# Kernel optimization log

Hardware: AMD Instinct MI355X
Metric: run time of the kernel (lower is better)

The kernel has to match this reference:

```python
import jax, jax.numpy as jnp
import numpy as np

N_EXPERTS = 8
K_ACTIVE = 2
D_MODEL = 512
D_FF = 2048
T = 4096  # batch * seq_len


def _xavier(key, shape, fan_in, fan_out):
    limit = np.sqrt(6.0 / (fan_in + fan_out))
    return jax.random.uniform(key, shape, jnp.float32, -limit, limit)


def setup_inputs() -> dict:
    key = jax.random.key(0)
    k1, k2, k3, k4, k5 = jax.random.split(key, 5)
    hidden_states = jax.random.normal(k1, (T, D_MODEL), jnp.float32)
    selected_experts = jax.random.randint(k2, (T, K_ACTIVE), 0, N_EXPERTS, jnp.int64)
    expert_masks = jax.random.uniform(k3, (T, N_EXPERTS), jnp.float32)
    # stacked expert weights; torch Linear computes x @ W.T, we store [E, in, out]
    W1 = _xavier(k4, (N_EXPERTS, D_MODEL, D_FF), D_MODEL, D_FF)
    W2 = _xavier(k5, (N_EXPERTS, D_FF, D_MODEL), D_FF, D_MODEL)
    return {
        "hidden_states": hidden_states,
        "selected_experts": selected_experts,
        "expert_masks": expert_masks,
        "W1": W1,
        "W2": W2,
    }


def reference(hidden_states, selected_experts, expert_masks, W1, W2):
    # hidden_states: [T, d_model]; selected_experts: [T, k]; W1: [E, d, f]; W2: [E, f, d]
    t, d = hidden_states.shape
    n_experts = W1.shape[0]
    k = selected_experts.shape[1]

    expert_outputs = jnp.zeros((t, k, d), dtype=hidden_states.dtype)
    for e in range(n_experts):  # fixed small expert set
        h = jax.nn.gelu(hidden_states @ W1[e], approximate=False)  # [T, d_ff]
        y = h @ W2[e]                                              # [T, d_model]
        mask = selected_experts == e                               # [T, k]; each (t,slot) matches exactly one e
        expert_outputs = jnp.where(mask[..., None], y[:, None, :], expert_outputs)

    # expert_loads[e] = (# (token, slot) assignments to e) / T, matching the torch loop
    flat = selected_experts.reshape(-1)
    expert_loads = jnp.zeros((n_experts,), jnp.float32).at[flat].add(1.0) / t
    return expert_outputs, expert_loads
```

## Files before the change

### kernel.cpp

```cpp
#include <hip/hip_runtime.h>
#include <hip/hip_bf16.h>


typedef __bf16 bf16x8 __attribute__((ext_vector_type(8)));
typedef float f32x4 __attribute__((ext_vector_type(4)));

#define DM 512
#define DF 2048
#define NE 8
#define NTOK 4096
#define NPAIR 8192
#define HCAP 9216

__device__ __forceinline__ unsigned short f2bf(float x) {
    unsigned u = __builtin_bit_cast(unsigned, x);
    return (unsigned short)((u + 0x7fffu + ((u >> 16) & 1u)) >> 16);
}
__device__ __forceinline__ unsigned pack2(float lo, float hi) {
    return (unsigned)f2bf(lo) | ((unsigned)f2bf(hi) << 16);
}
__device__ __forceinline__ float gelu_fast(float x) {
    float x2 = x * x;
    float z = x * __builtin_fmaf(x2, -0.1029432f, -2.3022083f);
    float e = __builtin_amdgcn_exp2f(z);
    return x * __builtin_amdgcn_rcpf(1.0f + e);
}
__device__ __forceinline__ void dma16(const unsigned short* g, unsigned short* l) {
    __builtin_amdgcn_global_load_lds(
        (const __attribute__((address_space(1))) void*)g,
        (__attribute__((address_space(3))) void*)l, 16, 0, 0);
}
__device__ __forceinline__ int slot64(int row, int c) { return row * 8 + (c ^ (row & 7)); }

__device__ __forceinline__ void mfma_step(const unsigned short* Ab, const unsigned short* Bb,
                                          int wm, int wn, int quad, int l15,
                                          f32x4 (&acc)[4][4]) {
#pragma unroll
    for (int kk = 0; kk < 2; ++kk) {
        const int c = kk * 4 + quad;
        bf16x8 a[4], b[4];
#pragma unroll
        for (int fm = 0; fm < 4; ++fm) {
            int row = wm * 64 + fm * 16 + l15;
            a[fm] = __builtin_bit_cast(bf16x8, *(const uint4*)&Ab[slot64(row, c) * 8]);
        }
#pragma unroll
        for (int fn = 0; fn < 4; ++fn) {
            int row = wn * 64 + fn * 16 + l15;
            b[fn] = __builtin_bit_cast(bf16x8, *(const uint4*)&Bb[slot64(row, c) * 8]);
        }
#pragma unroll
        for (int fm = 0; fm < 4; ++fm)
#pragma unroll
            for (int fn = 0; fn < 4; ++fn)
                acc[fm][fn] = __builtin_amdgcn_mfma_f32_16x16x32_bf16(a[fm], b[fn], acc[fm][fn], 0, 0, 0);
    }
}

#define STAGE(buf, ko)                                        \
    do {                                                      \
        _Pragma("unroll") for (int j_ = 0; j_ < 4; ++j_) {    \
            dma16(ga[j_] + (ko), la[j_] + (buf) * 8192);      \
            dma16(gb[j_] + (ko), lb[j_] + (buf) * 8192);      \
        }                                                     \
    } while (0)

#define WAITN(n)                                                  \
    do {                                                          \
        __builtin_amdgcn_sched_barrier(0);                        \
        asm volatile("s_waitcnt vmcnt(" #n ")" ::: "memory");     \
        __builtin_amdgcn_sched_barrier(0);                        \
    } while (0)

#define BAR() __builtin_amdgcn_s_barrier()

__global__ void k_prep(const float* __restrict__ X, unsigned short* __restrict__ Xb,
                       const float* __restrict__ W1, unsigned short* __restrict__ W1T,
                       const float* __restrict__ W2, unsigned short* __restrict__ W2T,
                       const int* __restrict__ sel, int* __restrict__ counts_g,
                       int* __restrict__ opad_g, int* __restrict__ rowmap,
                       float* __restrict__ loads_out) {
    __shared__ unsigned short T[64][65];
    __shared__ int hist[NE], cur[NE], off[NE];
    const int b = blockIdx.x, tid = threadIdx.x;

    if (b < 1024) {
        int i = (b * 256 + tid) * 8;
        float4 a = *(const float4*)(X + i);
        float4 c = *(const float4*)(X + i + 4);
        uint4 u;
        u.x = pack2(a.x, a.y); u.y = pack2(a.z, a.w);
        u.z = pack2(c.x, c.y); u.w = pack2(c.z, c.w);
        *(uint4*)(Xb + i) = u;
    } else if (b < 3072) {
        const int t = b - 1024;
        const int bx = t & 31, by = (t >> 5) & 7, bz = t >> 8;
        const int tx = tid & 15, ty = tid >> 4;
        const int r0 = by * 64, c0 = bx * 64;
        const float* src = W1 + ((size_t)bz * DM + r0) * DF + c0;
#pragma unroll
        for (int i = 0; i < 4; ++i) {
            int r = ty + i * 16;
            float4 v = *(const float4*)(src + (size_t)r * DF + tx * 4);
            T[tx * 4 + 0][r] = f2bf(v.x); T[tx * 4 + 1][r] = f2bf(v.y);
            T[tx * 4 + 2][r] = f2bf(v.z); T[tx * 4 + 3][r] = f2bf(v.w);
        }
        __syncthreads();
        unsigned short* dst = W1T + ((size_t)bz * DF + c0) * DM + r0;
#pragma unroll
        for (int i = 0; i < 4; ++i) {
            int c = ty + i * 16;
            ushort4 w;
            w.x = T[c][tx * 4 + 0]; w.y = T[c][tx * 4 + 1];
            w.z = T[c][tx * 4 + 2]; w.w = T[c][tx * 4 + 3];
            *(ushort4*)(dst + (size_t)c * DM + tx * 4) = w;
        }
    } else if (b == 3072) {
        if (tid < NE) { hist[tid] = 0; cur[tid] = 0; }
        __syncthreads();
#pragma unroll
        for (int i = 0; i < NPAIR / 256; ++i)
            atomicAdd(&hist[sel[i * 256 + tid]], 1);
        __syncthreads();
        if (tid == 0) {
            int s = 0;
            for (int e = 0; e < NE; ++e) {
                off[e] = s;
                s += (hist[e] + 127) & ~127;
                counts_g[e] = hist[e];
                opad_g[e] = off[e];
                loads_out[e] = (float)hist[e] * (1.0f / (float)NTOK);
            }
        }
        __syncthreads();
#pragma unroll
        for (int i = 0; i < NPAIR / 256; ++i) {
            int p = i * 256 + tid;
            int e = sel[p];
            int pos = atomicAdd(&cur[e], 1);
            rowmap[off[e] + pos] = p;
        }
    } else {
        const int t = b - 3073;
        const int bx = t & 7, by = (t >> 3) & 31, bz = t >> 8;
        const int tx = tid & 15, ty = tid >> 4;
        const int r0 = by * 64, c0 = bx * 64;
        const float* src = W2 + ((size_t)bz * DF + r0) * DM + c0;
#pragma unroll
        for (int i = 0; i < 4; ++i) {
            int r = ty + i * 16;
            float4 v = *(const float4*)(src + (size_t)r * DM + tx * 4);
            T[tx * 4 + 0][r] = f2bf(v.x); T[tx * 4 + 1][r] = f2bf(v.y);
            T[tx * 4 + 2][r] = f2bf(v.z); T[tx * 4 + 3][r] = f2bf(v.w);
        }
        __syncthreads();
        unsigned short* dst = W2T + ((size_t)bz * DM + c0) * DF + r0;
#pragma unroll
        for (int i = 0; i < 4; ++i) {
            int c = ty + i * 16;
            ushort4 w;
            w.x = T[c][tx * 4 + 0]; w.y = T[c][tx * 4 + 1];
            w.z = T[c][tx * 4 + 2]; w.w = T[c][tx * 4 + 3];
            *(ushort4*)(dst + (size_t)c * DF + tx * 4) = w;
        }
    }
}

__global__ void k_tw2(const float* __restrict__ in, unsigned short* __restrict__ out) {
    __shared__ unsigned short T[64][65];
    const int tid = threadIdx.x;
    const int tx = tid & 15, ty = tid >> 4;
    const int r0 = blockIdx.y * 64, c0 = blockIdx.x * 64;
    const float* src = in + ((size_t)blockIdx.z * DF + r0) * DM + c0;
#pragma unroll
    for (int i = 0; i < 4; ++i) {
        int r = ty + i * 16;
        float4 v = *(const float4*)(src + (size_t)r * DM + tx * 4);
        T[tx * 4 + 0][r] = f2bf(v.x); T[tx * 4 + 1][r] = f2bf(v.y);
        T[tx * 4 + 2][r] = f2bf(v.z); T[tx * 4 + 3][r] = f2bf(v.w);
    }
    __syncthreads();
    unsigned short* dst = out + ((size_t)blockIdx.z * DM + c0) * DF + r0;
#pragma unroll
    for (int i = 0; i < 4; ++i) {
        int c = ty + i * 16;
        ushort4 w;
        w.x = T[c][tx * 4 + 0]; w.y = T[c][tx * 4 + 1];
        w.z = T[c][tx * 4 + 2]; w.w = T[c][tx * 4 + 3];
        *(ushort4*)(dst + (size_t)c * DF + tx * 4) = w;
    }
}

__launch_bounds__(256, 2)
__global__ void k_gemm1d(const unsigned short* __restrict__ Xb,
                         const unsigned short* __restrict__ W1T,
                         const int* __restrict__ counts, const int* __restrict__ opad,
                         const int* __restrict__ rowmap, unsigned short* __restrict__ H) {
    const int e = blockIdx.z, mt = blockIdx.y, nt = blockIdx.x;
    const int grow = opad[e] + mt * 128;
    int valid = counts[e] - mt * 128;
    if (valid <= 0) return;
    if (valid > 128) valid = 128;

    __shared__ __align__(16) unsigned short SM[4][8192];
    __shared__ int toks[128];

    const int tid = threadIdx.x;
    if (tid < 128) {
        int i = (tid < valid) ? tid : 0;
        toks[tid] = rowmap[grow + i] >> 1;
    }
    __syncthreads();

    const int wave = tid >> 6, lane = tid & 63;
    const int wm = wave >> 1, wn = wave & 1;
    const int quad = lane >> 4, l15 = lane & 15;

    const unsigned short* ga[4];
    const unsigned short* gb[4];
    unsigned short* la[4];
    unsigned short* lb[4];
#pragma unroll
    for (int j = 0; j < 4; ++j) {
        int row = wave * 32 + j * 8 + (lane >> 3);
        int ch = (lane & 7) ^ ((lane >> 3) & 7);
        ga[j] = Xb + (size_t)toks[row] * DM + ch * 8;
        gb[j] = W1T + ((size_t)e * DF + nt * 128 + row) * DM + ch * 8;
        la[j] = &SM[0][(wave * 32 + j * 8) * 64];
        lb[j] = &SM[2][(wave * 32 + j * 8) * 64];
    }

    f32x4 acc[4][4] = {};

    STAGE(0, 0);
#pragma unroll 1
    for (int kt = 0; kt < 8; kt += 2) {
        if (kt + 1 < 8) { STAGE(1, (kt + 1) * 64); WAITN(8); } else { WAITN(0); }
        BAR();
        mfma_step(&SM[0][0], &SM[2][0], wm, wn, quad, l15, acc);
        BAR();
        if (kt + 2 < 8) { STAGE(0, (kt + 2) * 64); WAITN(8); } else { WAITN(0); }
        BAR();
        mfma_step(&SM[1][0], &SM[3][0], wm, wn, quad, l15, acc);
        BAR();
    }

    unsigned short* ep = &SM[0][0];
#pragma unroll
    for (int fm = 0; fm < 4; ++fm)
#pragma unroll
        for (int i = 0; i < 4; ++i) {
            int r = wm * 64 + fm * 16 + quad * 4 + i;
#pragma unroll
            for (int fn = 0; fn < 4; ++fn)
                ep[r * 136 + wn * 64 + fn * 16 + l15] = f2bf(gelu_fast(acc[fm][fn][i]));
        }
    __syncthreads();
    {
        const int rr0 = tid >> 4, ch = tid & 15;
#pragma unroll
        for (int it = 0; it < 8; ++it) {
            int r = it * 16 + rr0;
            uint4 v = *(const uint4*)&ep[r * 136 + ch * 8];
            *(uint4*)(H + (size_t)(grow + r) * DF + nt * 128 + ch * 8) = v;
        }
    }
}

__launch_bounds__(256, 2)
__global__ void k_gemm2d(const unsigned short* __restrict__ H,
                         const unsigned short* __restrict__ W2T,
                         const int* __restrict__ counts, const int* __restrict__ opad,
                         const int* __restrict__ rowmap, float* __restrict__ out) {
    const int e = blockIdx.z, mt = blockIdx.y, nt = blockIdx.x;
    const int grow = opad[e] + mt * 128;
    int valid = counts[e] - mt * 128;
    if (valid <= 0) return;
    if (valid > 128) valid = 128;

    __shared__ __align__(16) unsigned short As[2][128 * 64];
    __shared__ __align__(16) unsigned short Bs[2][128 * 64];
    __shared__ int pairs[128];

    const int tid = threadIdx.x;
    if (tid < 128) pairs[tid] = (tid < valid) ? rowmap[grow + tid] : 0;
    __syncthreads();

    const int wave = tid >> 6, lane = tid & 63;
    const int wm = wave >> 1, wn = wave & 1;
    const int quad = lane >> 4, l15 = lane & 15;

    const unsigned short* ga[4];
    const unsigned short* gb[4];
    unsigned short* la[4];
    unsigned short* lb[4];
#pragma unroll
    for (int j = 0; j < 4; ++j) {
        int row = wave * 32 + j * 8 + (lane >> 3);
        int ch = (lane & 7) ^ ((lane >> 3) & 7);
        int rr = (row < valid) ? row : 0;
        ga[j] = H + (size_t)(grow + rr) * DF + ch * 8;
        gb[j] = W2T + ((size_t)e * DM + nt * 128 + row) * DF + ch * 8;
        la[j] = &As[0][(wave * 32 + j * 8) * 64];
        lb[j] = &Bs[0][(wave * 32 + j * 8) * 64];
    }

    f32x4 acc[4][4] = {};

    STAGE(0, 0);
#pragma unroll 1
    for (int kt = 0; kt < 32; kt += 2) {
        if (kt + 1 < 32) { STAGE(1, (kt + 1) * 64); WAITN(8); } else { WAITN(0); }
        BAR();
        mfma_step(&As[0][0], &Bs[0][0], wm, wn, quad, l15, acc);
        BAR();
        if (kt + 2 < 32) { STAGE(0, (kt + 2) * 64); WAITN(8); } else { WAITN(0); }
        BAR();
        mfma_step(&As[1][0], &Bs[1][0], wm, wn, quad, l15, acc);
        BAR();
    }

#pragma unroll
    for (int fm = 0; fm < 4; ++fm) {
#pragma unroll
        for (int i = 0; i < 4; ++i) {
            int m_l = wm * 64 + fm * 16 + quad * 4 + i;
            if (m_l < valid) {
                float* orow = out + (size_t)pairs[m_l] * DM + nt * 128 + wn * 64;
#pragma unroll
                for (int fn = 0; fn < 4; ++fn)
                    orow[fn * 16 + l15] = acc[fm][fn][i];
            }
        }
    }
}

extern "C" void kernel_launch(void* const* d_in, const int* in_sizes, int n_in,
                              void* d_out, int out_size, void* d_ws, size_t ws_size,
                              hipStream_t stream) {
    const float* X = (const float*)d_in[0];
    const int* sel = (const int*)d_in[1];
    const float* W1 = (const float*)d_in[3];
    const float* W2 = (const float*)d_in[4];
    float* out = (float*)d_out;
    float* loads_out = out + (size_t)NPAIR * DM;

    int* counts = (int*)d_ws;
    int* opad = counts + 16;
    int* rowmap = counts + 32;
    const size_t hbytes = (size_t)HCAP * DF * 2;
    const size_t xbytes = (size_t)NTOK * DM * 2;
    const size_t w1tbytes = (size_t)NE * DF * DM * 2;
    unsigned short* H = (unsigned short*)((char*)d_ws + 65536);
    unsigned short* Xb = (unsigned short*)((char*)d_ws + 65536 + hbytes);
    unsigned short* WT = (unsigned short*)((char*)d_ws + 65536 + hbytes + xbytes);

    const bool fused = ws_size >= 65536 + hbytes + xbytes + 2 * w1tbytes;
    unsigned short* W2T = fused ? WT + w1tbytes / 2 : WT;

    hipLaunchKernelGGL(k_prep, dim3(fused ? 5121 : 3073), dim3(256), 0, stream,
                       X, Xb, W1, WT, W2, W2T, sel, counts, opad, rowmap, loads_out);
    hipLaunchKernelGGL(k_gemm1d, dim3(DF / 128, NPAIR / 128, NE), dim3(256), 0, stream,
                       Xb, WT, counts, opad, rowmap, H);
    if (!fused)
        hipLaunchKernelGGL(k_tw2, dim3(DM / 64, DF / 64, NE), dim3(256), 0, stream, W2, WT);
    hipLaunchKernelGGL(k_gemm2d, dim3(4, NPAIR / 128, NE), dim3(256), 0, stream,
                       H, W2T, counts, opad, rowmap, out);
}
```

Baseline: 195.6 us.

## Enlarge GEMM tiles to 256x256 and 128x256 with 512-thread blocks

The first grouped GEMM now uses 256x256 output tiles computed by 8 waves, each holding an 8x4 fragment accumulator. The second GEMM uses 128x256 tiles, also with 512 threads, and its A and B staging is resized to match. The goal is more reuse per LDS load and less redundant global traffic for activations and weights. In exchange, tile padding waste grows for experts with few tokens, the grid has fewer blocks, and register and LDS pressure rise, which may limit occupancy.

```diff
diff --git a/kernel.cpp b/kernel.cpp
--- a/kernel.cpp
+++ b/kernel.cpp
@@ -32,38 +32,27 @@
 }
 __device__ __forceinline__ int slot64(int row, int c) { return row * 8 + (c ^ (row & 7)); }
 
-__device__ __forceinline__ void mfma_step(const unsigned short* Ab, const unsigned short* Bb,
-                                          int wm, int wn, int quad, int l15,
-                                          f32x4 (&acc)[4][4]) {
+template<int FM>
+__device__ __forceinline__ void mfma_tileT(const unsigned short* Ab, const unsigned short* Bb,
+                                           int rbase, int cbase, int quad, int l15,
+                                           f32x4 (&acc)[FM][4]) {
 #pragma unroll
     for (int kk = 0; kk < 2; ++kk) {
         const int c = kk * 4 + quad;
-        bf16x8 a[4], b[4];
-#pragma unroll
-        for (int fm = 0; fm < 4; ++fm) {
-            int row = wm * 64 + fm * 16 + l15;
-            a[fm] = __builtin_bit_cast(bf16x8, *(const uint4*)&Ab[slot64(row, c) * 8]);
-        }
-#pragma unroll
-        for (int fn = 0; fn < 4; ++fn) {
-            int row = wn * 64 + fn * 16 + l15;
-            b[fn] = __builtin_bit_cast(bf16x8, *(const uint4*)&Bb[slot64(row, c) * 8]);
-        }
-#pragma unroll
-        for (int fm = 0; fm < 4; ++fm)
+        bf16x8 a[FM], b[4];
+#pragma unroll
+        for (int fm = 0; fm < FM; ++fm)
+            a[fm] = __builtin_bit_cast(bf16x8, *(const uint4*)&Ab[slot64(rbase + fm * 16 + l15, c) * 8]);
+#pragma unroll
+        for (int fn = 0; fn < 4; ++fn)
+            b[fn] = __builtin_bit_cast(bf16x8, *(const uint4*)&Bb[slot64(cbase + fn * 16 + l15, c) * 8]);
+#pragma unroll
+        for (int fm = 0; fm < FM; ++fm)
 #pragma unroll
             for (int fn = 0; fn < 4; ++fn)
                 acc[fm][fn] = __builtin_amdgcn_mfma_f32_16x16x32_bf16(a[fm], b[fn], acc[fm][fn], 0, 0, 0);
     }
 }
-
-#define STAGE(buf, ko)                                        \
-    do {                                                      \
-        _Pragma("unroll") for (int j_ = 0; j_ < 4; ++j_) {    \
-            dma16(ga[j_] + (ko), la[j_] + (buf) * 8192);      \
-            dma16(gb[j_] + (ko), lb[j_] + (buf) * 8192);      \
-        }                                                     \
-    } while (0)
 
 #define WAITN(n)                                                  \
     do {                                                          \
@@ -191,30 +180,40 @@
     }
 }
 
-__launch_bounds__(256, 2)
+#define STAGE1(buf, ko)                                        \
+    do {                                                       \
+        _Pragma("unroll") for (int j_ = 0; j_ < 4; ++j_) {     \
+            dma16(ga[j_] + (ko), la[j_] + (buf) * 16384);      \
+            dma16(gb[j_] + (ko), lb[j_] + (buf) * 16384);      \
+        }                                                      \
+    } while (0)
+
+__launch_bounds__(512, 2)
 __global__ void k_gemm1d(const unsigned short* __restrict__ Xb,
                          const unsigned short* __restrict__ W1T,
                          const int* __restrict__ counts, const int* __restrict__ opad,
                          const int* __restrict__ rowmap, unsigned short* __restrict__ H) {
     const int e = blockIdx.z, mt = blockIdx.y, nt = blockIdx.x;
-    const int grow = opad[e] + mt * 128;
-    int valid = counts[e] - mt * 128;
+    const int grow = opad[e] + mt * 256;
+    int valid = counts[e] - mt * 256;
     if (valid <= 0) return;
-    if (valid > 128) valid = 128;
-
-    __shared__ __align__(16) unsigned short SM[4][8192];
-    __shared__ int toks[128];
+    if (valid > 256) valid = 256;
+
+    __shared__ __align__(16) unsigned char SMRAW[256 * 272 * 2];
+    __shared__ int toks[256];
+    unsigned short* As = (unsigned short*)SMRAW;
+    unsigned short* Bs = As + 32768;
 
     const int tid = threadIdx.x;
-    if (tid < 128) {
+    if (tid < 256) {
         int i = (tid < valid) ? tid : 0;
         toks[tid] = rowmap[grow + i] >> 1;
     }
     __syncthreads();
 
     const int wave = tid >> 6, lane = tid & 63;
-    const int wm = wave >> 1, wn = wave & 1;
     const int quad = lane >> 4, l15 = lane & 15;
+    const int rbase = (wave >> 2) * 128, cbase = (wave & 3) * 64;
 
     const unsigned short* ga[4];
     const unsigned short* gb[4];
@@ -222,52 +221,64 @@
     unsigned short* lb[4];
 #pragma unroll
     for (int j = 0; j < 4; ++j) {
-        int row = wave * 32 + j * 8 + (lane >> 3);
-        int ch = (lane & 7) ^ ((lane >> 3) & 7);
+        int slot = wave * 256 + j * 64 + lane;
+        int row = slot >> 3;
+        int ch = (slot & 7) ^ (row & 7);
         ga[j] = Xb + (size_t)toks[row] * DM + ch * 8;
-        gb[j] = W1T + ((size_t)e * DF + nt * 128 + row) * DM + ch * 8;
-        la[j] = &SM[0][(wave * 32 + j * 8) * 64];
-        lb[j] = &SM[2][(wave * 32 + j * 8) * 64];
-    }
-
-    f32x4 acc[4][4] = {};
-
-    STAGE(0, 0);
+        gb[j] = W1T + ((size_t)e * DF + nt * 256 + row) * DM + ch * 8;
+        la[j] = As + (wave * 256 + j * 64) * 8;
+        lb[j] = Bs + (wave * 256 + j * 64) * 8;
+    }
+
+    f32x4 acc[8][4] = {};
+
+    STAGE1(0, 0);
 #pragma unroll 1
     for (int kt = 0; kt < 8; kt += 2) {
-        if (kt + 1 < 8) { STAGE(1, (kt + 1) * 64); WAITN(8); } else { WAITN(0); }
-        BAR();
-        mfma_step(&SM[0][0], &SM[2][0], wm, wn, quad, l15, acc);
-        BAR();
-        if (kt + 2 < 8) { STAGE(0, (kt + 2) * 64); WAITN(8); } else { WAITN(0); }
-        BAR();
-        mfma_step(&SM[1][0], &SM[3][0], wm, wn, quad, l15, acc);
-        BAR();
-    }
-
-    unsigned short* ep = &SM[0][0];
-#pragma unroll
-    for (int fm = 0; fm < 4; ++fm)
-#pragma unroll
-        for (int i = 0; i < 4; ++i) {
-            int r = wm * 64 + fm * 16 + quad * 4 + i;
+        if (kt + 1 < 8) { STAGE1(1, (kt + 1) * 64); WAITN(8); } else { WAITN(0); }
+        BAR();
+        mfma_tileT<8>(As, Bs, rbase, cbase, quad, l15, acc);
+        BAR();
+        if (kt + 2 < 8) { STAGE1(0, (kt + 2) * 64); WAITN(8); } else { WAITN(0); }
+        BAR();
+        mfma_tileT<8>(As + 16384, Bs + 16384, rbase, cbase, quad, l15, acc);
+        BAR();
+    }
+
+    unsigned short* ep = (unsigned short*)SMRAW;
+#pragma unroll
+    for (int fm = 0; fm < 8; ++fm)
+#pragma unroll
+        for (int i = 0; i < 4; ++i) {
+            int r = rbase + fm * 16 + quad * 4 + i;
 #pragma unroll
             for (int fn = 0; fn < 4; ++fn)
-                ep[r * 136 + wn * 64 + fn * 16 + l15] = f2bf(gelu_fast(acc[fm][fn][i]));
+                ep[r * 272 + cbase + fn * 16 + l15] = f2bf(gelu_fast(acc[fm][fn][i]));
         }
     __syncthreads();
     {
-        const int rr0 = tid >> 4, ch = tid & 15;
-#pragma unroll
-        for (int it = 0; it < 8; ++it) {
-            int r = it * 16 + rr0;
-            uint4 v = *(const uint4*)&ep[r * 136 + ch * 8];
-            *(uint4*)(H + (size_t)(grow + r) * DF + nt * 128 + ch * 8) = v;
-        }
-    }
-}
-
-__launch_bounds__(256, 2)
+        const int pvalid = (valid + 127) & ~127;
+        const int ch = tid & 31, rr = tid >> 5;
+#pragma unroll
+        for (int it = 0; it < 16; ++it) {
+            int r = it * 16 + rr;
+            if (r < pvalid) {
+                uint4 v = *(const uint4*)&ep[r * 272 + ch * 8];
+                *(uint4*)(H + (size_t)(grow + r) * DF + nt * 256 + ch * 8) = v;
+            }
+        }
+    }
+}
+
+#define STAGE2(buf, ko)                                        \
+    do {                                                       \
+        _Pragma("unroll") for (int j_ = 0; j_ < 2; ++j_)       \
+            dma16(ga[j_] + (ko), la[j_] + (buf) * 8192);       \
+        _Pragma("unroll") for (int j_ = 0; j_ < 4; ++j_)       \
+            dma16(gb[j_] + (ko), lb[j_] + (buf) * 16384);      \
+    } while (0)
+
+__launch_bounds__(512, 2)
 __global__ void k_gemm2d(const unsigned short* __restrict__ H,
                          const unsigned short* __restrict__ W2T,
                          const int* __restrict__ counts, const int* __restrict__ opad,
@@ -278,8 +289,8 @@
     if (valid <= 0) return;
     if (valid > 128) valid = 128;
 
-    __shared__ __align__(16) unsigned short As[2][128 * 64];
-    __shared__ __align__(16) unsigned short Bs[2][128 * 64];
+    __shared__ __align__(16) unsigned short As2[2][8192];
+    __shared__ __align__(16) unsigned short Bs2[2][16384];
     __shared__ int pairs[128];
 
     const int tid = threadIdx.x;
@@ -287,36 +298,43 @@
     __syncthreads();
 
     const int wave = tid >> 6, lane = tid & 63;
-    const int wm = wave >> 1, wn = wave & 1;
     const int quad = lane >> 4, l15 = lane & 15;
-
-    const unsigned short* ga[4];
-    const unsigned short* gb[4];
-    unsigned short* la[4];
-    unsigned short* lb[4];
-#pragma unroll
-    for (int j = 0; j < 4; ++j) {
-        int row = wave * 32 + j * 8 + (lane >> 3);
-        int ch = (lane & 7) ^ ((lane >> 3) & 7);
+    const int rbase = (wave >> 2) * 64, cbase = (wave & 3) * 64;
+
+    const unsigned short* ga[2];
+    unsigned short* la[2];
+#pragma unroll
+    for (int j = 0; j < 2; ++j) {
+        int slot = wave * 128 + j * 64 + lane;
+        int row = slot >> 3;
+        int ch = (slot & 7) ^ (row & 7);
         int rr = (row < valid) ? row : 0;
         ga[j] = H + (size_t)(grow + rr) * DF + ch * 8;
-        gb[j] = W2T + ((size_t)e * DM + nt * 128 + row) * DF + ch * 8;
-        la[j] = &As[0][(wave * 32 + j * 8) * 64];
-        lb[j] = &Bs[0][(wave * 32 + j * 8) * 64];
+        la[j] = &As2[0][(wave * 128 + j * 64) * 8];
+    }
+    const unsigned short* gb[4];
+    unsigned short* lb[4];
+#pragma unroll
+    for (int j = 0; j < 4; ++j) {
+        int slot = wave * 256 + j * 64 + lane;
+        int row = slot >> 3;
+        int ch = (slot & 7) ^ (row & 7);
+        gb[j] = W2T + ((size_t)e * DM + nt * 256 + row) * DF + ch * 8;
+        lb[j] = &Bs2[0][(wave * 256 + j * 64) * 8];
     }
 
     f32x4 acc[4][4] = {};
 
-    STAGE(0, 0);
+    STAGE2(0, 0);
 #pragma unroll 1
     for (int kt = 0; kt < 32; kt += 2) {
-        if (kt + 1 < 32) { STAGE(1, (kt + 1) * 64); WAITN(8); } else { WAITN(0); }
-        BAR();
-        mfma_step(&As[0][0], &Bs[0][0], wm, wn, quad, l15, acc);
-        BAR();
-        if (kt + 2 < 32) { STAGE(0, (kt + 2) * 64); WAITN(8); } else { WAITN(0); }
-        BAR();
-        mfma_step(&As[1][0], &Bs[1][0], wm, wn, quad, l15, acc);
+        if (kt + 1 < 32) { STAGE2(1, (kt + 1) * 64); WAITN(6); } else { WAITN(0); }
+        BAR();
+        mfma_tileT<4>(&As2[0][0], &Bs2[0][0], rbase, cbase, quad, l15, acc);
+        BAR();
+        if (kt + 2 < 32) { STAGE2(0, (kt + 2) * 64); WAITN(6); } else { WAITN(0); }
+        BAR();
+        mfma_tileT<4>(&As2[1][0], &Bs2[1][0], rbase, cbase, quad, l15, acc);
         BAR();
     }
 
@@ -324,9 +342,9 @@
     for (int fm = 0; fm < 4; ++fm) {
 #pragma unroll
         for (int i = 0; i < 4; ++i) {
-            int m_l = wm * 64 + fm * 16 + quad * 4 + i;
+            int m_l = rbase + fm * 16 + quad * 4 + i;
             if (m_l < valid) {
-                float* orow = out + (size_t)pairs[m_l] * DM + nt * 128 + wn * 64;
+                float* orow = out + (size_t)pairs[m_l] * DM + nt * 256 + cbase;
 #pragma unroll
                 for (int fn = 0; fn < 4; ++fn)
                     orow[fn * 16 + l15] = acc[fm][fn][i];
@@ -360,10 +378,10 @@
 
     hipLaunchKernelGGL(k_prep, dim3(fused ? 5121 : 3073), dim3(256), 0, stream,
                        X, Xb, W1, WT, W2, W2T, sel, counts, opad, rowmap, loads_out);
-    hipLaunchKernelGGL(k_gemm1d, dim3(DF / 128, NPAIR / 128, NE), dim3(256), 0, stream,
+    hipLaunchKernelGGL(k_gemm1d, dim3(DF / 256, NPAIR / 256, NE), dim3(512), 0, stream,
                        Xb, WT, counts, opad, rowmap, H);
     if (!fused)
         hipLaunchKernelGGL(k_tw2, dim3(DM / 64, DF / 64, NE), dim3(256), 0, stream, W2, WT);
-    hipLaunchKernelGGL(k_gemm2d, dim3(4, NPAIR / 128, NE), dim3(256), 0, stream,
+    hipLaunchKernelGGL(k_gemm2d, dim3(DM / 256, NPAIR / 128, NE), dim3(512), 0, stream,
                        H, W2T, counts, opad, rowmap, out);
 }
```

Result: slower. 214.4 us (+9.6%).
